# Optimization experiments

Hardware: AMD Instinct MI355X
Metric: run time of the kernel (lower is better)

The kernel has to match this reference:

```python
import jax, jax.numpy as jnp
import numpy as np
import math

D_MODEL = 1024
N_HEADS = 16
GEOM_DIM = 7
B, S = 4, 1024


def setup_inputs() -> dict:
    key = jax.random.key(0)
    ks = jax.random.split(key, 12)
    w = lambda k, shape: (jax.random.normal(k, shape, dtype=jnp.float32) * 0.02)
    return {
        "x": jax.random.normal(ks[0], (B, S, D_MODEL), dtype=jnp.float32),
        "geom_feat": jax.random.normal(ks[1], (B, S, S, GEOM_DIM), dtype=jnp.float32),
        "mask": jax.random.randint(ks[2], (B, S), 0, 2, dtype=jnp.int32),
        "Wq": w(ks[3], (D_MODEL, D_MODEL)), "bq": jnp.zeros((D_MODEL,), jnp.float32),
        "Wk": w(ks[4], (D_MODEL, D_MODEL)), "bk": jnp.zeros((D_MODEL,), jnp.float32),
        "Wv": w(ks[5], (D_MODEL, D_MODEL)), "bv": jnp.zeros((D_MODEL,), jnp.float32),
        "Wo": w(ks[6], (D_MODEL, D_MODEL)), "bo": jnp.zeros((D_MODEL,), jnp.float32),
        "Wg": w(ks[7], (GEOM_DIM, N_HEADS)), "bg": jnp.zeros((N_HEADS,), jnp.float32),
    }


def reference(x, geom_feat, mask, Wq, bq, Wk, bk, Wv, bv, Wo, bo, Wg, bg):
    b, s, d = x.shape
    h = Wg.shape[1]
    dk = d // h
    scale = math.sqrt(dk)
    # QKV projections -> [b, h, s, dk]
    Q = (x @ Wq + bq).reshape(b, s, h, dk).transpose(0, 2, 1, 3)
    K = (x @ Wk + bk).reshape(b, s, h, dk).transpose(0, 2, 1, 3)
    V = (x @ Wv + bv).reshape(b, s, h, dk).transpose(0, 2, 1, 3)
    # attention scores [b, h, s, s]
    scores = jnp.einsum("bhqd,bhkd->bhqk", Q, K) / scale
    # geometric structure bias: [b,s,s,geom_dim] -> [b,s,s,h] -> [b,h,s,s]
    struct_bias = (geom_feat @ Wg + bg).transpose(0, 3, 1, 2)
    scores = scores + struct_bias
    # key-padding mask [b, s] -> [b, 1, 1, s]
    scores = jnp.where(mask[:, None, None, :] == 0, -10000.0, scores)
    attn = jax.nn.softmax(scores, axis=-1)  # dropout disabled (eval / p=0)
    ctx = jnp.einsum("bhqk,bhkd->bhqd", attn, V)
    ctx = ctx.transpose(0, 2, 1, 3).reshape(b, s, d)
    return ctx @ Wo + bo
```

## Files before the change

kernel.cpp:

```cpp
#include <hip/hip_runtime.h>
#include <hip/hip_bf16.h>
#include <math.h>

#define BB 4
#define SS 1024
#define DD 1024
#define NH 16
#define DK 64
#define GD 7

typedef _Float16 half8 __attribute__((ext_vector_type(8)));
typedef _Float16 half4v __attribute__((ext_vector_type(4)));
typedef float floatx4 __attribute__((ext_vector_type(4)));

__device__ inline half8 cvt8(const float4 a, const float4 b) {
  half8 h;
  h[0] = (_Float16)a.x; h[1] = (_Float16)a.y; h[2] = (_Float16)a.z; h[3] = (_Float16)a.w;
  h[4] = (_Float16)b.x; h[5] = (_Float16)b.y; h[6] = (_Float16)b.z; h[7] = (_Float16)b.w;
  return h;
}

__global__ __launch_bounds__(256) void cvtx(const float* __restrict__ x,
                                            _Float16* __restrict__ xh) {
  const int i = blockIdx.x * 256 + threadIdx.x;
  const float4 a = ((const float4*)x)[i * 2];
  const float4 b = ((const float4*)x)[i * 2 + 1];
  ((half8*)xh)[i] = cvt8(a, b);
}

__global__ __launch_bounds__(256) void packw(const float* __restrict__ Wq,
                                             const float* __restrict__ Wk,
                                             const float* __restrict__ Wv,
                                             const float* __restrict__ Wo,
                                             _Float16* __restrict__ Wt) {
  __shared__ _Float16 Tl[64 * 72];
  const int t = threadIdx.x;
  const int k0 = blockIdx.x * 64, n0 = blockIdx.y * 64, z = blockIdx.z;
  const float* src = (z == 0) ? Wq : (z == 1) ? Wk : (z == 2) ? Wv : Wo;
#pragma unroll
  for (int i = 0; i < 4; ++i) {
    const int u = i * 256 + t;
    const int r = u >> 4, c4 = (u & 15) * 4;
    const float4 v = *(const float4*)(src + (size_t)(k0 + r) * DD + n0 + c4);
    Tl[(c4 + 0) * 72 + r] = (_Float16)v.x;
    Tl[(c4 + 1) * 72 + r] = (_Float16)v.y;
    Tl[(c4 + 2) * 72 + r] = (_Float16)v.z;
    Tl[(c4 + 3) * 72 + r] = (_Float16)v.w;
  }
  __syncthreads();
  _Float16* dst = Wt + (size_t)z * DD * DD;
#pragma unroll
  for (int i = 0; i < 2; ++i) {
    const int u = i * 256 + t;
    const int nr = u >> 3, ks = u & 7;
    const half8 hv = *(const half8*)&Tl[nr * 72 + ks * 8];
    *(half8*)(dst + (size_t)(n0 + nr) * DD + k0 + ks * 8) = hv;
  }
}

__global__ __launch_bounds__(256) void biasprep(const float* __restrict__ geom,
                                                const int* __restrict__ mask,
                                                const float* __restrict__ Wg,
                                                const float* __restrict__ bg,
                                                _Float16* __restrict__ bias16) {
  __shared__ float wgL[GD * NH + NH];
  const int t = threadIdx.x;
  const int q = blockIdx.x, b = blockIdx.y;
  if (t < GD * NH) wgL[t] = Wg[t];
  if (t < NH) wgL[GD * NH + t] = bg[t];

  const float* gp = geom + ((size_t)b * SS + q) * SS * GD + (size_t)t * 28;
  float4 gv[7];
#pragma unroll
  for (int i = 0; i < 7; ++i) gv[i] = *(const float4*)(gp + i * 4);
  const float* gf = (const float*)gv;

  const int4 m4 = *(const int4*)(mask + b * SS + t * 4);
  const int mk[4] = {m4.x, m4.y, m4.z, m4.w};

  __syncthreads();

  _Float16* dst = bias16 + ((size_t)b * NH * SS + q) * SS + t * 4;
#pragma unroll
  for (int h = 0; h < NH; ++h) {
    float wg[GD];
#pragma unroll
    for (int g = 0; g < GD; ++g) wg[g] = wgL[g * NH + h];
    const float bgh = wgL[GD * NH + h];
    half4v hv;
#pragma unroll
    for (int k2 = 0; k2 < 4; ++k2) {
      float bi = bgh;
#pragma unroll
      for (int g = 0; g < GD; ++g) bi = fmaf(gf[k2 * GD + g], wg[g], bi);
      hv[k2] = mk[k2] ? (_Float16)bi : (_Float16)(-100.f);
    }
    *(half4v*)(dst + (size_t)h * SS * SS) = hv;
  }
}

template <int MODE>
__global__ __launch_bounds__(256) void hgemm(const _Float16* __restrict__ A,
                                             const _Float16* __restrict__ Bt,
                                             const float* __restrict__ b0,
                                             const float* __restrict__ b1,
                                             const float* __restrict__ b2,
                                             _Float16* __restrict__ Oq,
                                             _Float16* __restrict__ Ok,
                                             _Float16* __restrict__ Ov,
                                             float* __restrict__ Of) {
  __shared__ _Float16 Als[128 * 72];
  __shared__ _Float16 Bls[128 * 72];
  const int t = threadIdx.x;
  const int w = t >> 6, lane = t & 63, quad = lane >> 4, col = lane & 15;
  const int m0 = blockIdx.x * 128, n0 = blockIdx.y * 128;
  const int mw = (w >> 1) * 64, nw = (w & 1) * 64;
  const floatx4 zero4 = {0.f, 0.f, 0.f, 0.f};
  floatx4 acc[4][4];
#pragma unroll
  for (int i = 0; i < 4; ++i)
#pragma unroll
    for (int j = 0; j < 4; ++j) acc[i][j] = zero4;

  for (int k0 = 0; k0 < DD; k0 += 64) {
#pragma unroll
    for (int i = 0; i < 4; ++i) {
      const int u = i * 256 + t;
      const int row = u >> 3, seg = u & 7;
      const half8 hv = *(const half8*)(A + (size_t)(m0 + row) * DD + k0 + seg * 8);
      *(half8*)&Als[row * 72 + seg * 8] = hv;
    }
#pragma unroll
    for (int i = 0; i < 4; ++i) {
      const int u = i * 256 + t;
      const int row = u >> 3, seg = u & 7;
      const half8 hv = *(const half8*)(Bt + (size_t)(n0 + row) * DD + k0 + seg * 8);
      *(half8*)&Bls[row * 72 + seg * 8] = hv;
    }
    __syncthreads();
#pragma unroll
    for (int kk = 0; kk < 2; ++kk) {
      half8 af[4], bf[4];
      const int u = (quad + kk * 4) * 8;
#pragma unroll
      for (int i = 0; i < 4; ++i) af[i] = *(const half8*)&Als[(mw + i * 16 + col) * 72 + u];
#pragma unroll
      for (int j = 0; j < 4; ++j) bf[j] = *(const half8*)&Bls[(nw + j * 16 + col) * 72 + u];
#pragma unroll
      for (int i = 0; i < 4; ++i)
#pragma unroll
        for (int j = 0; j < 4; ++j)
          acc[i][j] = __builtin_amdgcn_mfma_f32_16x16x32_f16(af[i], bf[j], acc[i][j], 0, 0, 0);
    }
    __syncthreads();
  }

#pragma unroll
  for (int j = 0; j < 4; ++j) {
    const int n = n0 + nw + j * 16 + col;
    if (MODE == 0) {
      const int which = n >> 10, hd = n & 1023;
      const int h = hd >> 6, d = hd & 63;
      const float* bp = (which == 0) ? b0 : (which == 1) ? b1 : b2;
      const float bias = bp[hd];
      _Float16* ob = (which == 0) ? Oq : (which == 1) ? Ok : Ov;
#pragma unroll
      for (int i = 0; i < 4; ++i) {
#pragma unroll
        for (int reg = 0; reg < 4; ++reg) {
          const int m = m0 + mw + i * 16 + quad * 4 + reg;
          const int b = m >> 10, s = m & 1023;
          ob[(((size_t)b * NH + h) * SS + s) * DK + d] = (_Float16)(acc[i][j][reg] + bias);
        }
      }
    } else {
      const float bias = b0[n];
#pragma unroll
      for (int i = 0; i < 4; ++i) {
#pragma unroll
        for (int reg = 0; reg < 4; ++reg) {
          const int m = m0 + mw + i * 16 + quad * 4 + reg;
          Of[(size_t)m * DD + n] = acc[i][j][reg] + bias;
        }
      }
    }
  }
}

template <bool PREBIAS>
__global__ __launch_bounds__(256) void attn(const _Float16* __restrict__ Q,
                                            const _Float16* __restrict__ K,
                                            const _Float16* __restrict__ V,
                                            const _Float16* __restrict__ bias16,
                                            const float* __restrict__ geom,
                                            const int* __restrict__ mask,
                                            const float* __restrict__ Wg,
                                            const float* __restrict__ bg,
                                            _Float16* __restrict__ ctxbuf) {
  __shared__ _Float16 Ks[64 * 64];
  __shared__ _Float16 Vt[64 * 72];
  __shared__ _Float16 biasL[64 * 72];
  __shared__ _Float16 pL[4 * 16 * 72];
  __shared__ unsigned char mskL[SS];

  const int t = threadIdx.x;
  const int w = t >> 6, lane = t & 63, quad = lane >> 4, col = lane & 15;
  const int h = blockIdx.x, qt = blockIdx.y, b = blockIdx.z;
  const int q0 = qt * 64;
  const size_t bh = (size_t)b * NH + h;
  const _Float16* Qb = Q + bh * SS * DK;
  const _Float16* Kb = K + bh * SS * DK;
  const _Float16* Vb = V + bh * SS * DK;

  {
    const int j = t >> 2, u2 = (t & 3) * 2;
    const half8 h0 = *(const half8*)(Qb + (size_t)(q0 + j) * DK + u2 * 8);
    const half8 h1 = *(const half8*)(Qb + (size_t)(q0 + j) * DK + u2 * 8 + 8);
    *(half8*)&Ks[(j * 8 + (u2 ^ (j & 7))) * 8] = h0;
    *(half8*)&Ks[(j * 8 + ((u2 + 1) ^ (j & 7))) * 8] = h1;
  }
  if constexpr (!PREBIAS) {
    const int4 m4 = *(const int4*)(mask + b * SS + t * 4);
    mskL[t * 4 + 0] = m4.x != 0;
    mskL[t * 4 + 1] = m4.y != 0;
    mskL[t * 4 + 2] = m4.z != 0;
    mskL[t * 4 + 3] = m4.w != 0;
  }
  __syncthreads();
  half8 qfrag[2];
  {
    const int qrow = w * 16 + col;
#pragma unroll
    for (int kk = 0; kk < 2; ++kk) {
      const int u = quad + kk * 4;
      qfrag[kk] = *(const half8*)&Ks[(qrow * 8 + (u ^ (qrow & 7))) * 8];
    }
  }

  float wgv[GD];
  float bgh = 0.f;
  const float* gptr = nullptr;
  if constexpr (!PREBIAS) {
#pragma unroll
    for (int g = 0; g < GD; ++g) wgv[g] = Wg[g * NH + h];
    bgh = bg[h];
    gptr = geom + (((size_t)b * SS + (q0 + (t >> 2))) * SS + (t & 3) * 16) * GD;
  }
  const _Float16* bbase = nullptr;
  if constexpr (PREBIAS) bbase = bias16 + (bh * SS + q0) * SS;

  const floatx4 zero4 = {0.f, 0.f, 0.f, 0.f};
  floatx4 ctx[4] = {zero4, zero4, zero4, zero4};
  float lsum[4] = {0.f, 0.f, 0.f, 0.f};
  _Float16* pW = &pL[w * 16 * 72];

  for (int c = 0; c < 16; ++c) {
    const int k0 = c * 64;
    __syncthreads();

    {
      const int j = t >> 2, u2 = (t & 3) * 2;
      const half8 h0 = *(const half8*)(Kb + (size_t)(k0 + j) * DK + u2 * 8);
      const half8 h1 = *(const half8*)(Kb + (size_t)(k0 + j) * DK + u2 * 8 + 8);
      *(half8*)&Ks[(j * 8 + (u2 ^ (j & 7))) * 8] = h0;
      *(half8*)&Ks[(j * 8 + ((u2 + 1) ^ (j & 7))) * 8] = h1;
    }
    {
      const int kg = (t >> 4) * 4, dg = (t & 15) * 4;
      half4v f[4];
#pragma unroll
      for (int e = 0; e < 4; ++e)
        f[e] = *(const half4v*)(Vb + (size_t)(k0 + kg + e) * DK + dg);
#pragma unroll
      for (int i = 0; i < 4; ++i) {
        half4v hv = {f[0][i], f[1][i], f[2][i], f[3][i]};
        *(half4v*)&Vt[(dg + i) * 72 + kg] = hv;
      }
    }
    if constexpr (PREBIAS) {
#pragma unroll
      for (int i = 0; i < 2; ++i) {
        const int u2 = t * 2 + i;
        const int row = u2 >> 3, seg = u2 & 7;
        const half8 hv = *(const half8*)(bbase + (size_t)row * SS + k0 + seg * 8);
        *(half8*)&biasL[row * 72 + seg * 8] = hv;
      }
    } else {
      const int gq = t >> 2, gk = (t & 3) * 16;
#pragma unroll
      for (int sg = 0; sg < 4; ++sg) {
        float4 gv[7];
#pragma unroll
        for (int i7 = 0; i7 < 7; ++i7) gv[i7] = *(const float4*)(gptr + sg * 28 + i7 * 4);
        const float* gf = (const float*)gv;
        half4v bv;
#pragma unroll
        for (int k2 = 0; k2 < 4; ++k2) {
          float bi = bgh;
#pragma unroll
          for (int g = 0; g < GD; ++g) bi = fmaf(gf[k2 * GD + g], wgv[g], bi);
          bv[k2] = mskL[k0 + gk + sg * 4 + k2] ? (_Float16)bi : (_Float16)(-100.f);
        }
        *(half4v*)&biasL[gq * 72 + gk + sg * 4] = bv;
      }
      gptr += 64 * GD;
    }
    __syncthreads();

    floatx4 sc[4] = {zero4, zero4, zero4, zero4};
#pragma unroll
    for (int nt = 0; nt < 4; ++nt) {
      const int key = nt * 16 + col;
#pragma unroll
      for (int kk = 0; kk < 2; ++kk) {
        const int u = quad + kk * 4;
        const half8 kf = *(const half8*)&Ks[(key * 8 + (u ^ (key & 7))) * 8];
        sc[nt] = __builtin_amdgcn_mfma_f32_16x16x32_f16(qfrag[kk], kf, sc[nt], 0, 0, 0);
      }
    }

#pragma unroll
    for (int nt = 0; nt < 4; ++nt) {
#pragma unroll
      for (int reg = 0; reg < 4; ++reg) {
        const int q = quad * 4 + reg;
        const float s =
            fmaf(sc[nt][reg], 0.125f, (float)biasL[(w * 16 + q) * 72 + nt * 16 + col]);
        const float p = __expf(s);
        lsum[reg] += p;
        pW[q * 72 + nt * 16 + col] = (_Float16)p;
      }
    }

#pragma unroll
    for (int kk = 0; kk < 2; ++kk) {
      const half8 pa = *(const half8*)&pW[col * 72 + quad * 8 + kk * 32];
#pragma unroll
      for (int nt = 0; nt < 4; ++nt) {
        const half8 vb = *(const half8*)&Vt[(nt * 16 + col) * 72 + quad * 8 + kk * 32];
        ctx[nt] = __builtin_amdgcn_mfma_f32_16x16x32_f16(pa, vb, ctx[nt], 0, 0, 0);
      }
    }
  }

  float inv[4];
#pragma unroll
  for (int reg = 0; reg < 4; ++reg) {
    float l = lsum[reg];
    l += __shfl_xor(l, 1, 64);
    l += __shfl_xor(l, 2, 64);
    l += __shfl_xor(l, 4, 64);
    l += __shfl_xor(l, 8, 64);
    inv[reg] = 1.f / l;
  }
#pragma unroll
  for (int nt = 0; nt < 4; ++nt) {
#pragma unroll
    for (int reg = 0; reg < 4; ++reg) {
      const int q = q0 + w * 16 + quad * 4 + reg;
      ctxbuf[((size_t)b * SS + q) * DD + h * DK + nt * 16 + col] =
          (_Float16)(ctx[nt][reg] * inv[reg]);
    }
  }
}

extern "C" void kernel_launch(void* const* d_in, const int* in_sizes, int n_in,
                              void* d_out, int out_size, void* d_ws, size_t ws_size,
                              hipStream_t stream) {
  const float* x    = (const float*)d_in[0];
  const float* geom = (const float*)d_in[1];
  const int*   mask = (const int*)d_in[2];
  const float* Wq   = (const float*)d_in[3];
  const float* bq   = (const float*)d_in[4];
  const float* Wk   = (const float*)d_in[5];
  const float* bk   = (const float*)d_in[6];
  const float* Wv   = (const float*)d_in[7];
  const float* bv   = (const float*)d_in[8];
  const float* Wo   = (const float*)d_in[9];
  const float* bo   = (const float*)d_in[10];
  const float* Wg   = (const float*)d_in[11];
  const float* bg   = (const float*)d_in[12];
  float* out = (float*)d_out;

  const size_t NEL = (size_t)BB * SS * DD;
  char* p = (char*)d_ws;
  _Float16* xh   = (_Float16*)p;            p += NEL * 2;
  _Float16* Wt   = (_Float16*)p;            p += NEL * 2;
  _Float16* Qh   = (_Float16*)p;            p += NEL * 2;
  _Float16* Kh   = (_Float16*)p;            p += NEL * 2;
  _Float16* Vh   = (_Float16*)p;            p += NEL * 2;
  _Float16* ctxh = (_Float16*)p;            p += NEL * 2;
  _Float16* bias16 = (_Float16*)p;
  const size_t need = (size_t)48 * 1024 * 1024 + (size_t)BB * NH * SS * SS * 2;
  const bool prebias = ws_size >= need;

  cvtx<<<2048, 256, 0, stream>>>(x, xh);
  packw<<<dim3(16, 16, 4), 256, 0, stream>>>(Wq, Wk, Wv, Wo, Wt);
  if (prebias)
    biasprep<<<dim3(SS, BB), 256, 0, stream>>>(geom, mask, Wg, bg, bias16);

  hgemm<0><<<dim3(32, 24), 256, 0, stream>>>(xh, Wt, bq, bk, bv, Qh, Kh, Vh, nullptr);

  if (prebias)
    attn<true><<<dim3(NH, SS / 64, BB), 256, 0, stream>>>(Qh, Kh, Vh, bias16, geom, mask,
                                                          Wg, bg, ctxh);
  else
    attn<false><<<dim3(NH, SS / 64, BB), 256, 0, stream>>>(Qh, Kh, Vh, nullptr, geom, mask,
                                                           Wg, bg, ctxh);

  hgemm<1><<<dim3(32, 8), 256, 0, stream>>>(ctxh, Wt + (size_t)3 * DD * DD, bo, nullptr,
                                            nullptr, nullptr, nullptr, nullptr, out);
}
```

Baseline: 369.1 us.

## Merge prep kernels and co-schedule QKV GEMM with geometric bias precompute

Merges the x conversion and weight packing kernels into one launch. Puts the QKV projection GEMM and the geometric-bias/mask precompute into a single kernel, with blocks picking their role from the block index. The bias precompute now handles 8 keys per thread with 16-byte stores. The aim is fewer launches and running the memory-bound bias pass alongside the compute-bound GEMM. The cost is a larger combined LDS footprint per block, which may lower occupancy.

```diff
diff --git a/kernel.cpp b/kernel.cpp
--- a/kernel.cpp
+++ b/kernel.cpp
@@ -20,22 +20,25 @@
   return h;
 }
 
-__global__ __launch_bounds__(256) void cvtx(const float* __restrict__ x,
-                                            _Float16* __restrict__ xh) {
-  const int i = blockIdx.x * 256 + threadIdx.x;
-  const float4 a = ((const float4*)x)[i * 2];
-  const float4 b = ((const float4*)x)[i * 2 + 1];
-  ((half8*)xh)[i] = cvt8(a, b);
-}
-
-__global__ __launch_bounds__(256) void packw(const float* __restrict__ Wq,
-                                             const float* __restrict__ Wk,
-                                             const float* __restrict__ Wv,
-                                             const float* __restrict__ Wo,
-                                             _Float16* __restrict__ Wt) {
+__global__ __launch_bounds__(256) void prep(const float* __restrict__ x,
+                                            _Float16* __restrict__ xh,
+                                            const float* __restrict__ Wq,
+                                            const float* __restrict__ Wk,
+                                            const float* __restrict__ Wv,
+                                            const float* __restrict__ Wo,
+                                            _Float16* __restrict__ Wt) {
   __shared__ _Float16 Tl[64 * 72];
   const int t = threadIdx.x;
-  const int k0 = blockIdx.x * 64, n0 = blockIdx.y * 64, z = blockIdx.z;
+  if (blockIdx.x < 2048) {
+    const int i = blockIdx.x * 256 + t;
+    const float4 a = ((const float4*)x)[i * 2];
+    const float4 b = ((const float4*)x)[i * 2 + 1];
+    ((half8*)xh)[i] = cvt8(a, b);
+    return;
+  }
+  const int pf = blockIdx.x - 2048;
+  const int z = pf >> 8, rem = pf & 255;
+  const int n0 = (rem >> 4) * 64, k0 = (rem & 15) * 64;
   const float* src = (z == 0) ? Wq : (z == 1) ? Wk : (z == 2) ? Wv : Wo;
 #pragma unroll
   for (int i = 0; i < 4; ++i) {
@@ -58,57 +61,136 @@
   }
 }
 
-__global__ __launch_bounds__(256) void biasprep(const float* __restrict__ geom,
-                                                const int* __restrict__ mask,
-                                                const float* __restrict__ Wg,
-                                                const float* __restrict__ bg,
-                                                _Float16* __restrict__ bias16) {
-  __shared__ float wgL[GD * NH + NH];
+template <bool PRE>
+__global__ __launch_bounds__(256) void fused0(const _Float16* __restrict__ A,
+                                              const _Float16* __restrict__ Bt,
+                                              const float* __restrict__ bq,
+                                              const float* __restrict__ bk,
+                                              const float* __restrict__ bv,
+                                              _Float16* __restrict__ Oq,
+                                              _Float16* __restrict__ Ok,
+                                              _Float16* __restrict__ Ov,
+                                              const float* __restrict__ geom,
+                                              const int* __restrict__ mask,
+                                              const float* __restrict__ Wg,
+                                              const float* __restrict__ bg,
+                                              _Float16* __restrict__ bias16) {
   const int t = threadIdx.x;
-  const int q = blockIdx.x, b = blockIdx.y;
-  if (t < GD * NH) wgL[t] = Wg[t];
-  if (t < NH) wgL[GD * NH + t] = bg[t];
-
-  const float* gp = geom + ((size_t)b * SS + q) * SS * GD + (size_t)t * 28;
-  float4 gv[7];
-#pragma unroll
-  for (int i = 0; i < 7; ++i) gv[i] = *(const float4*)(gp + i * 4);
-  const float* gf = (const float*)gv;
-
-  const int4 m4 = *(const int4*)(mask + b * SS + t * 4);
-  const int mk[4] = {m4.x, m4.y, m4.z, m4.w};
-
-  __syncthreads();
-
-  _Float16* dst = bias16 + ((size_t)b * NH * SS + q) * SS + t * 4;
-#pragma unroll
-  for (int h = 0; h < NH; ++h) {
-    float wg[GD];
-#pragma unroll
-    for (int g = 0; g < GD; ++g) wg[g] = wgL[g * NH + h];
-    const float bgh = wgL[GD * NH + h];
-    half4v hv;
-#pragma unroll
-    for (int k2 = 0; k2 < 4; ++k2) {
-      float bi = bgh;
-#pragma unroll
-      for (int g = 0; g < GD; ++g) bi = fmaf(gf[k2 * GD + g], wg[g], bi);
-      hv[k2] = mk[k2] ? (_Float16)bi : (_Float16)(-100.f);
-    }
-    *(half4v*)(dst + (size_t)h * SS * SS) = hv;
-  }
-}
-
-template <int MODE>
-__global__ __launch_bounds__(256) void hgemm(const _Float16* __restrict__ A,
-                                             const _Float16* __restrict__ Bt,
-                                             const float* __restrict__ b0,
-                                             const float* __restrict__ b1,
-                                             const float* __restrict__ b2,
-                                             _Float16* __restrict__ Oq,
-                                             _Float16* __restrict__ Ok,
-                                             _Float16* __restrict__ Ov,
-                                             float* __restrict__ Of) {
+  if (blockIdx.x < 768) {
+    __shared__ _Float16 Als[128 * 72];
+    __shared__ _Float16 Bls[128 * 72];
+    const int w = t >> 6, lane = t & 63, quad = lane >> 4, col = lane & 15;
+    const int m0 = (blockIdx.x & 31) * 128, n0 = (blockIdx.x >> 5) * 128;
+    const int mw = (w >> 1) * 64, nw = (w & 1) * 64;
+    const floatx4 zero4 = {0.f, 0.f, 0.f, 0.f};
+    floatx4 acc[4][4];
+#pragma unroll
+    for (int i = 0; i < 4; ++i)
+#pragma unroll
+      for (int j = 0; j < 4; ++j) acc[i][j] = zero4;
+
+    for (int k0 = 0; k0 < DD; k0 += 64) {
+#pragma unroll
+      for (int i = 0; i < 4; ++i) {
+        const int u = i * 256 + t;
+        const int row = u >> 3, seg = u & 7;
+        const half8 hv = *(const half8*)(A + (size_t)(m0 + row) * DD + k0 + seg * 8);
+        *(half8*)&Als[row * 72 + seg * 8] = hv;
+      }
+#pragma unroll
+      for (int i = 0; i < 4; ++i) {
+        const int u = i * 256 + t;
+        const int row = u >> 3, seg = u & 7;
+        const half8 hv = *(const half8*)(Bt + (size_t)(n0 + row) * DD + k0 + seg * 8);
+        *(half8*)&Bls[row * 72 + seg * 8] = hv;
+      }
+      __syncthreads();
+#pragma unroll
+      for (int kk = 0; kk < 2; ++kk) {
+        half8 af[4], bf[4];
+        const int u = (quad + kk * 4) * 8;
+#pragma unroll
+        for (int i = 0; i < 4; ++i)
+          af[i] = *(const half8*)&Als[(mw + i * 16 + col) * 72 + u];
+#pragma unroll
+        for (int j = 0; j < 4; ++j)
+          bf[j] = *(const half8*)&Bls[(nw + j * 16 + col) * 72 + u];
+#pragma unroll
+        for (int i = 0; i < 4; ++i)
+#pragma unroll
+          for (int j = 0; j < 4; ++j)
+            acc[i][j] =
+                __builtin_amdgcn_mfma_f32_16x16x32_f16(af[i], bf[j], acc[i][j], 0, 0, 0);
+      }
+      __syncthreads();
+    }
+
+#pragma unroll
+    for (int j = 0; j < 4; ++j) {
+      const int n = n0 + nw + j * 16 + col;
+      const int which = n >> 10, hd = n & 1023;
+      const int h = hd >> 6, d = hd & 63;
+      const float* bp = (which == 0) ? bq : (which == 1) ? bk : bv;
+      const float bias = bp[hd];
+      _Float16* ob = (which == 0) ? Oq : (which == 1) ? Ok : Ov;
+#pragma unroll
+      for (int i = 0; i < 4; ++i) {
+#pragma unroll
+        for (int reg = 0; reg < 4; ++reg) {
+          const int m = m0 + mw + i * 16 + quad * 4 + reg;
+          const int b = m >> 10, s = m & 1023;
+          ob[(((size_t)b * NH + h) * SS + s) * DK + d] = (_Float16)(acc[i][j][reg] + bias);
+        }
+      }
+    }
+    return;
+  }
+
+  if constexpr (PRE) {
+    __shared__ float wgL[GD * NH + NH];
+    const int r = blockIdx.x - 768;
+    const int b = r >> 9;
+    const int q = (r & 511) * 2 + (t >> 7);
+    const int k8 = (t & 127) * 8;
+    if (t < GD * NH) wgL[t] = Wg[t];
+    if (t < NH) wgL[GD * NH + t] = bg[t];
+
+    const float* gp = geom + ((size_t)b * SS + q) * SS * GD + (size_t)k8 * GD;
+    float4 gv[14];
+#pragma unroll
+    for (int i = 0; i < 14; ++i) gv[i] = *(const float4*)(gp + i * 4);
+    const float* gf = (const float*)gv;
+
+    const int4 m4a = *(const int4*)(mask + b * SS + k8);
+    const int4 m4b = *(const int4*)(mask + b * SS + k8 + 4);
+    const int mk[8] = {m4a.x, m4a.y, m4a.z, m4a.w, m4b.x, m4b.y, m4b.z, m4b.w};
+
+    __syncthreads();
+
+    _Float16* dst = bias16 + ((size_t)b * NH * SS + q) * SS + k8;
+#pragma unroll
+    for (int h = 0; h < NH; ++h) {
+      float wg[GD];
+#pragma unroll
+      for (int g = 0; g < GD; ++g) wg[g] = wgL[g * NH + h];
+      const float bgh = wgL[GD * NH + h];
+      half8 hv;
+#pragma unroll
+      for (int k2 = 0; k2 < 8; ++k2) {
+        float bi = bgh;
+#pragma unroll
+        for (int g = 0; g < GD; ++g) bi = fmaf(gf[k2 * GD + g], wg[g], bi);
+        hv[k2] = mk[k2] ? (_Float16)bi : (_Float16)(-100.f);
+      }
+      *(half8*)(dst + (size_t)h * SS * SS) = hv;
+    }
+  }
+}
+
+__global__ __launch_bounds__(256) void hgemm1(const _Float16* __restrict__ A,
+                                              const _Float16* __restrict__ Bt,
+                                              const float* __restrict__ b0,
+                                              float* __restrict__ Of) {
   __shared__ _Float16 Als[128 * 72];
   __shared__ _Float16 Bls[128 * 72];
   const int t = threadIdx.x;
@@ -158,30 +240,13 @@
 #pragma unroll
   for (int j = 0; j < 4; ++j) {
     const int n = n0 + nw + j * 16 + col;
-    if (MODE == 0) {
-      const int which = n >> 10, hd = n & 1023;
-      const int h = hd >> 6, d = hd & 63;
-      const float* bp = (which == 0) ? b0 : (which == 1) ? b1 : b2;
-      const float bias = bp[hd];
-      _Float16* ob = (which == 0) ? Oq : (which == 1) ? Ok : Ov;
-#pragma unroll
-      for (int i = 0; i < 4; ++i) {
-#pragma unroll
-        for (int reg = 0; reg < 4; ++reg) {
-          const int m = m0 + mw + i * 16 + quad * 4 + reg;
-          const int b = m >> 10, s = m & 1023;
-          ob[(((size_t)b * NH + h) * SS + s) * DK + d] = (_Float16)(acc[i][j][reg] + bias);
-        }
-      }
-    } else {
-      const float bias = b0[n];
-#pragma unroll
-      for (int i = 0; i < 4; ++i) {
-#pragma unroll
-        for (int reg = 0; reg < 4; ++reg) {
-          const int m = m0 + mw + i * 16 + quad * 4 + reg;
-          Of[(size_t)m * DD + n] = acc[i][j][reg] + bias;
-        }
+    const float bias = b0[n];
+#pragma unroll
+    for (int i = 0; i < 4; ++i) {
+#pragma unroll
+      for (int reg = 0; reg < 4; ++reg) {
+        const int m = m0 + mw + i * 16 + quad * 4 + reg;
+        Of[(size_t)m * DD + n] = acc[i][j][reg] + bias;
       }
     }
   }
@@ -394,20 +459,19 @@
   const size_t need = (size_t)48 * 1024 * 1024 + (size_t)BB * NH * SS * SS * 2;
   const bool prebias = ws_size >= need;
 
-  cvtx<<<2048, 256, 0, stream>>>(x, xh);
-  packw<<<dim3(16, 16, 4), 256, 0, stream>>>(Wq, Wk, Wv, Wo, Wt);
-  if (prebias)
-    biasprep<<<dim3(SS, BB), 256, 0, stream>>>(geom, mask, Wg, bg, bias16);
-
-  hgemm<0><<<dim3(32, 24), 256, 0, stream>>>(xh, Wt, bq, bk, bv, Qh, Kh, Vh, nullptr);
-
-  if (prebias)
+  prep<<<3072, 256, 0, stream>>>(x, xh, Wq, Wk, Wv, Wo, Wt);
+
+  if (prebias) {
+    fused0<true><<<768 + 2048, 256, 0, stream>>>(xh, Wt, bq, bk, bv, Qh, Kh, Vh,
+                                                 geom, mask, Wg, bg, bias16);
     attn<true><<<dim3(NH, SS / 64, BB), 256, 0, stream>>>(Qh, Kh, Vh, bias16, geom, mask,
                                                           Wg, bg, ctxh);
-  else
+  } else {
+    fused0<false><<<768, 256, 0, stream>>>(xh, Wt, bq, bk, bv, Qh, Kh, Vh,
+                                           geom, mask, Wg, bg, nullptr);
     attn<false><<<dim3(NH, SS / 64, BB), 256, 0, stream>>>(Qh, Kh, Vh, nullptr, geom, mask,
                                                            Wg, bg, ctxh);
-
-  hgemm<1><<<dim3(32, 8), 256, 0, stream>>>(ctxh, Wt + (size_t)3 * DD * DD, bo, nullptr,
-                                            nullptr, nullptr, nullptr, nullptr, out);
-}
+  }
+
+  hgemm1<<<dim3(32, 8), 256, 0, stream>>>(ctxh, Wt + (size_t)3 * DD * DD, bo, out);
+}
```

Result: no change. 363.2 us (-1.6%).
